# Kernel optimization log

Hardware: AMD Instinct MI355X
Metric: run time of the kernel (lower is better)

## Reference

```python
import jax, jax.numpy as jnp
import numpy as np

B, L, D, Y = 8, 2500, 512, 8921


def setup_inputs() -> dict:
    key = jax.random.key(0)
    k1, k2, k3, k4, k5, k6 = jax.random.split(key, 6)
    x = jax.random.normal(k1, (B, L, D), dtype=jnp.float32)
    target = jax.random.uniform(k2, (B, Y), dtype=jnp.float32)
    text_inputs = jax.random.randint(k3, (B, L), 0, 50000, dtype=jnp.int32)
    # Xavier-uniform-like init for the two [Y, D] weights
    lim = float(np.sqrt(6.0 / (Y + D)))
    U_weight = jax.random.uniform(k4, (Y, D), dtype=jnp.float32, minval=-lim, maxval=lim)
    final_weight = jax.random.uniform(k5, (Y, D), dtype=jnp.float32, minval=-lim, maxval=lim)
    final_bias = jax.random.uniform(k6, (Y,), dtype=jnp.float32, minval=-0.05, maxval=0.05)
    return {"x": x, "target": target, "text_inputs": text_inputs,
            "U_weight": U_weight, "final_weight": final_weight, "final_bias": final_bias}


def reference(x, target, text_inputs, U_weight, final_weight, final_bias):
    # att: [B, Y, L] = U.weight @ x^T
    att = jnp.einsum('yd,bld->byl', U_weight, x)
    # softmax over sequence dim
    alpha = jax.nn.softmax(att, axis=2)
    # per-label context: [B, Y, D]
    m = jnp.einsum('byl,bld->byd', alpha, x)
    # gated reduction instead of a linear layer: [B, Y]
    y = jnp.einsum('byd,yd->by', m, final_weight) + final_bias
    # BCEWithLogitsLoss (mean over all elements), numerically stable
    loss = jnp.mean(jnp.maximum(y, 0.0) - y * target + jnp.log1p(jnp.exp(-jnp.abs(y))))
    return (y, loss)
```

## Files before the change

kernel.cpp:

```cpp
#include <hip/hip_runtime.h>
#include <stdint.h>

#define B_ 8
#define L_ 2500
#define D_ 512
#define Y_ 8921
#define LP 2560
#define YP 8960
#define BLK 128
#define BK 32
#define NKT 16
#define NS 4
#define LTS 5

typedef float f32x4 __attribute__((ext_vector_type(4)));
typedef __bf16 bf16x8 __attribute__((ext_vector_type(8)));
typedef unsigned short u16;
typedef unsigned int u32;

__device__ __forceinline__ u32 pack2(float a, float b) {
  u32 ua = __float_as_uint(a); ua = (ua + 0x7FFFu + ((ua >> 16) & 1u)) >> 16;
  u32 ub = __float_as_uint(b); ub = (ub + 0x7FFFu + ((ub >> 16) & 1u)) >> 16;
  return ua | (ub << 16);
}

__global__ void cvt_x_kernel(const float* __restrict__ x, u16* __restrict__ xb) {
  int idx = blockIdx.x * 256 + threadIdx.x;
  int row = idx >> 6;
  int c8  = (idx & 63) << 3;
  int b = row / LP;
  int l = row - b * LP;
  uint4 o;
  if (l < L_) {
    const float* s = x + (size_t)(b * L_ + l) * D_ + c8;
    float4 f0 = *(const float4*)s;
    float4 f1 = *(const float4*)(s + 4);
    o.x = pack2(f0.x, f0.y); o.y = pack2(f0.z, f0.w);
    o.z = pack2(f1.x, f1.y); o.w = pack2(f1.z, f1.w);
  } else {
    o = make_uint4(0u, 0u, 0u, 0u);
  }
  *(uint4*)(xb + (size_t)row * D_ + c8) = o;
}

__global__ void cvt_w_kernel(const float* __restrict__ U, const float* __restrict__ Wf,
                             u16* __restrict__ Ub, u16* __restrict__ Wb) {
  int idx = blockIdx.x * 256 + threadIdx.x;
  const int half = YP * 64;
  const float* src = U; u16* dst = Ub;
  int i = idx;
  if (idx >= half) { i -= half; src = Wf; dst = Wb; }
  int row = i >> 6;
  int c8  = (i & 63) << 3;
  uint4 o;
  if (row < Y_) {
    const float* s = src + (size_t)row * D_ + c8;
    float4 f0 = *(const float4*)s;
    float4 f1 = *(const float4*)(s + 4);
    o.x = pack2(f0.x, f0.y); o.y = pack2(f0.z, f0.w);
    o.z = pack2(f1.x, f1.y); o.w = pack2(f1.z, f1.w);
  } else {
    o = make_uint4(0u, 0u, 0u, 0u);
  }
  *(uint4*)(dst + (size_t)row * D_ + c8) = o;
}

__device__ __forceinline__ void async16(const u16* g, u16* l) {
  __builtin_amdgcn_global_load_lds(
      (const __attribute__((address_space(1))) u32*)g,
      (__attribute__((address_space(3))) u32*)l, 16, 0, 0);
}

__global__ __launch_bounds__(256, 2) void fused_kernel(
    const u16* __restrict__ xb,
    const u16* __restrict__ Ub,
    const u16* __restrict__ Wb,
    float* __restrict__ part)
{
  __shared__ __align__(16) u16 sU[BLK * BK];
  __shared__ __align__(16) u16 sW[BLK * BK];
  __shared__ __align__(16) u16 sX[BLK * BK];

  const int t    = threadIdx.x;
  const int lane = t & 63;
  const int wv   = t >> 6;
  const int l16  = lane & 15;
  const int q    = lane >> 4;
  const int b    = blockIdx.y;
  const int y0   = blockIdx.x * BLK;
  const int s    = blockIdx.z;

  const int srow = t >> 2;
  const int scol = (t & 3) << 3;
  const u16* gU0 = Ub + (size_t)(y0 + srow) * D_ + scol;
  const u16* gU1 = gU0 + (size_t)64 * D_;
  const u16* gW0 = Wb + (size_t)(y0 + srow) * D_ + scol;
  const u16* gW1 = gW0 + (size_t)64 * D_;
  const u16* gXb = xb + (size_t)b * LP * D_ + (size_t)srow * D_ + scol;
  u16* lU0 = sU + t * 8;  u16* lU1 = sU + 2048 + t * 8;
  u16* lW0 = sW + t * 8;  u16* lW1 = sW + 2048 + t * 8;
  u16* lX0 = sX + t * 8;  u16* lX1 = sX + 2048 + t * 8;

  float M[8], Z[8], W[8];
#pragma unroll
  for (int i = 0; i < 8; ++i) { M[i] = -1e30f; Z[i] = 0.f; W[i] = 0.f; }

  const f32x4 z4 = {0.f, 0.f, 0.f, 0.f};

  for (int ltl = 0; ltl < LTS; ++ltl) {
    const int l0 = (s * LTS + ltl) * BLK;
    const u16* gX0 = gXb + (size_t)l0 * D_;
    const u16* gX1 = gX0 + (size_t)64 * D_;

    f32x4 accA[2][8], accS[2][8];
#pragma unroll
    for (int ry = 0; ry < 2; ++ry)
#pragma unroll
      for (int cl = 0; cl < 8; ++cl) { accA[ry][cl] = z4; accS[ry][cl] = z4; }

    for (int kt = 0; kt < NKT; ++kt) {
      const int ko = kt * BK;
      __syncthreads();
      async16(gU0 + ko, lU0);
      async16(gU1 + ko, lU1);
      async16(gW0 + ko, lW0);
      async16(gW1 + ko, lW1);
      async16(gX0 + ko, lX0);
      async16(gX1 + ko, lX1);
      __syncthreads();

      bf16x8 aU0 = *(const bf16x8*)(const void*)(sU + (wv * 32 + l16) * BK + q * 8);
      bf16x8 aU1 = *(const bf16x8*)(const void*)(sU + (wv * 32 + 16 + l16) * BK + q * 8);
      bf16x8 aW0 = *(const bf16x8*)(const void*)(sW + (wv * 32 + l16) * BK + q * 8);
      bf16x8 aW1 = *(const bf16x8*)(const void*)(sW + (wv * 32 + 16 + l16) * BK + q * 8);
#pragma unroll
      for (int cl = 0; cl < 8; ++cl) {
        bf16x8 bX = *(const bf16x8*)(const void*)(sX + (cl * 16 + l16) * BK + q * 8);
        accA[0][cl] = __builtin_amdgcn_mfma_f32_16x16x32_bf16(aU0, bX, accA[0][cl], 0, 0, 0);
        accA[1][cl] = __builtin_amdgcn_mfma_f32_16x16x32_bf16(aU1, bX, accA[1][cl], 0, 0, 0);
        accS[0][cl] = __builtin_amdgcn_mfma_f32_16x16x32_bf16(aW0, bX, accS[0][cl], 0, 0, 0);
        accS[1][cl] = __builtin_amdgcn_mfma_f32_16x16x32_bf16(aW1, bX, accS[1][cl], 0, 0, 0);
      }
    }

    const bool boundary = (l0 + BLK > L_);
#pragma unroll
    for (int ry = 0; ry < 2; ++ry) {
#pragma unroll
      for (int r = 0; r < 4; ++r) {
        const int si = ry * 4 + r;
        float a[8];
        if (boundary) {
#pragma unroll
          for (int cl = 0; cl < 8; ++cl) {
            float v = accA[ry][cl][r];
            a[cl] = (l0 + cl * 16 + l16 >= L_) ? -1e30f : v;
          }
        } else {
#pragma unroll
          for (int cl = 0; cl < 8; ++cl) a[cl] = accA[ry][cl][r];
        }
        float tmax = a[0];
#pragma unroll
        for (int cl = 1; cl < 8; ++cl) tmax = fmaxf(tmax, a[cl]);
        const float mnew  = fmaxf(M[si], tmax);
        const float scale = __expf(M[si] - mnew);
        float zl = 0.f, wl = 0.f;
#pragma unroll
        for (int cl = 0; cl < 8; ++cl) {
          float p = __expf(a[cl] - mnew);
          zl += p;
          wl = fmaf(p, accS[ry][cl][r], wl);
        }
        Z[si] = fmaf(Z[si], scale, zl);
        W[si] = fmaf(W[si], scale, wl);
        M[si] = mnew;
      }
    }
  }

#pragma unroll
  for (int si = 0; si < 8; ++si) {
    float M0 = M[si], Z0 = Z[si], W0 = W[si];
#pragma unroll
    for (int st = 1; st <= 8; st <<= 1) {
      const float Mo = __shfl_xor(M0, st);
      const float Zo = __shfl_xor(Z0, st);
      const float Wo = __shfl_xor(W0, st);
      const float mn = fmaxf(M0, Mo);
      const float sa = __expf(M0 - mn);
      const float sb = __expf(Mo - mn);
      Z0 = Z0 * sa + Zo * sb;
      W0 = W0 * sa + Wo * sb;
      M0 = mn;
    }
    M[si] = M0; Z[si] = Z0; W[si] = W0;
  }

  if (l16 == 0) {
    float* p = part + ((size_t)(b * 70 + blockIdx.x) * NS + s) * 384;
#pragma unroll
    for (int ry = 0; ry < 2; ++ry) {
#pragma unroll
      for (int r = 0; r < 4; ++r) {
        const int si = ry * 4 + r;
        const int yl = wv * 32 + ry * 16 + q * 4 + r;
        p[yl]       = M[si];
        p[128 + yl] = Z[si];
        p[256 + yl] = W[si];
      }
    }
  }
}

__global__ void combine_kernel(const float* __restrict__ part,
                               const float* __restrict__ bias,
                               const float* __restrict__ target,
                               float* __restrict__ out) {
  const int idx = blockIdx.x * 256 + threadIdx.x;
  float lpart = 0.f;
  if (idx < B_ * Y_) {
    const int b = idx / Y_;
    const int y = idx - b * Y_;
    const int yt = y >> 7, yl = y & 127;
    const float* p = part + ((size_t)(b * 70 + yt) * NS) * 384 + yl;
    float M = -1e30f;
#pragma unroll
    for (int s2 = 0; s2 < NS; ++s2) M = fmaxf(M, p[s2 * 384]);
    float Z = 0.f, W = 0.f;
#pragma unroll
    for (int s2 = 0; s2 < NS; ++s2) {
      const float e = __expf(p[s2 * 384] - M);
      Z = fmaf(p[s2 * 384 + 128], e, Z);
      W = fmaf(p[s2 * 384 + 256], e, W);
    }
    const float yv = W / Z + bias[y];
    out[idx] = yv;
    const float tg = target[idx];
    lpart = fmaxf(yv, 0.f) - yv * tg + log1pf(__expf(-fabsf(yv)));
  }
  lpart += __shfl_xor(lpart, 1);  lpart += __shfl_xor(lpart, 2);
  lpart += __shfl_xor(lpart, 4);  lpart += __shfl_xor(lpart, 8);
  lpart += __shfl_xor(lpart, 16); lpart += __shfl_xor(lpart, 32);
  if ((threadIdx.x & 63) == 0)
    atomicAdd(out + (size_t)B_ * Y_, lpart * (1.0f / (B_ * Y_)));
}

extern "C" void kernel_launch(void* const* d_in, const int* in_sizes, int n_in,
                              void* d_out, int out_size, void* d_ws, size_t ws_size,
                              hipStream_t stream) {
  const float* x      = (const float*)d_in[0];
  const float* target = (const float*)d_in[1];
  const float* U      = (const float*)d_in[3];
  const float* Wf     = (const float*)d_in[4];
  const float* bias   = (const float*)d_in[5];
  float* out = (float*)d_out;

  u16* xb = (u16*)d_ws;
  u16* Ub = xb + (size_t)B_ * LP * D_;
  u16* Wb = Ub + (size_t)YP * D_;
  float* part = (float*)(Wb + (size_t)YP * D_);

  hipMemsetAsync(out + (size_t)B_ * Y_, 0, sizeof(float), stream);
  cvt_x_kernel<<<dim3((B_ * LP * 64) / 256), 256, 0, stream>>>(x, xb);
  cvt_w_kernel<<<dim3((2 * YP * 64) / 256), 256, 0, stream>>>(U, Wf, Ub, Wb);
  fused_kernel<<<dim3(YP / BLK, B_, NS), 256, 0, stream>>>(xb, Ub, Wb, part);
  combine_kernel<<<dim3((B_ * Y_ + 255) / 256), 256, 0, stream>>>(part, bias, target, out);
}
```

Before: 575.7 us.

## Double-buffer LDS tiles and prefetch next k-step across sequence tiles

Shared-memory tiles for U, W and x are doubled. Each iteration issues the async global-to-LDS loads for the next k-step, which can cross into the next sequence tile, before computing on the current buffer. A manual vmcnt wait and barriers replace the two syncthreads per step, and MFMA sections run at raised wave priority. The aim is to hide global load latency behind the matrix math, at the cost of twice the LDS footprint, which may reduce occupancy.

```diff
diff --git a/kernel.cpp b/kernel.cpp
--- a/kernel.cpp
+++ b/kernel.cpp
@@ -12,6 +12,7 @@
 #define NKT 16
 #define NS 4
 #define LTS 5
+#define TOT (LTS * NKT)
 
 typedef float f32x4 __attribute__((ext_vector_type(4)));
 typedef __bf16 bf16x8 __attribute__((ext_vector_type(8)));
@@ -77,9 +78,9 @@
     const u16* __restrict__ Wb,
     float* __restrict__ part)
 {
-  __shared__ __align__(16) u16 sU[BLK * BK];
-  __shared__ __align__(16) u16 sW[BLK * BK];
-  __shared__ __align__(16) u16 sX[BLK * BK];
+  __shared__ __align__(16) u16 sU[2][BLK * BK];
+  __shared__ __align__(16) u16 sW[2][BLK * BK];
+  __shared__ __align__(16) u16 sX[2][BLK * BK];
 
   const int t    = threadIdx.x;
   const int lane = t & 63;
@@ -97,9 +98,6 @@
   const u16* gW0 = Wb + (size_t)(y0 + srow) * D_ + scol;
   const u16* gW1 = gW0 + (size_t)64 * D_;
   const u16* gXb = xb + (size_t)b * LP * D_ + (size_t)srow * D_ + scol;
-  u16* lU0 = sU + t * 8;  u16* lU1 = sU + 2048 + t * 8;
-  u16* lW0 = sW + t * 8;  u16* lW1 = sW + 2048 + t * 8;
-  u16* lX0 = sX + t * 8;  u16* lX1 = sX + 2048 + t * 8;
 
   float M[8], Z[8], W[8];
 #pragma unroll
@@ -107,42 +105,62 @@
 
   const f32x4 z4 = {0.f, 0.f, 0.f, 0.f};
 
+  auto stage = [&](int stp, int bf) {
+    const int kt = stp & (NKT - 1);
+    const int lt = stp >> 4;
+    const int ko = kt * BK;
+    const u16* gX = gXb + (size_t)((s * LTS + lt) * BLK) * D_ + ko;
+    async16(gU0 + ko, &sU[bf][t * 8]);
+    async16(gU1 + ko, &sU[bf][2048 + t * 8]);
+    async16(gW0 + ko, &sW[bf][t * 8]);
+    async16(gW1 + ko, &sW[bf][2048 + t * 8]);
+    async16(gX,                  &sX[bf][t * 8]);
+    async16(gX + (size_t)64 * D_, &sX[bf][2048 + t * 8]);
+  };
+
+  stage(0, 0);
+
+  int step = 0;
   for (int ltl = 0; ltl < LTS; ++ltl) {
+    f32x4 accA[2][8], accS[2][8];
+#pragma unroll
+    for (int ry = 0; ry < 2; ++ry)
+#pragma unroll
+      for (int cl = 0; cl < 8; ++cl) { accA[ry][cl] = z4; accS[ry][cl] = z4; }
+
+    for (int kt = 0; kt < NKT; ++kt, ++step) {
+      const int nstep = step + 1;
+      if (nstep < TOT) stage(nstep, nstep & 1);
+
+      if (nstep < TOT) asm volatile("s_waitcnt vmcnt(6)" ::: "memory");
+      else             asm volatile("s_waitcnt vmcnt(0)" ::: "memory");
+      __builtin_amdgcn_s_barrier();
+      asm volatile("" ::: "memory");
+
+      const int cb = step & 1;
+      const u16* bU = sU[cb];
+      const u16* bW = sW[cb];
+      const u16* bX = sX[cb];
+
+      bf16x8 aU0 = *(const bf16x8*)(const void*)(bU + (wv * 32 + l16) * BK + q * 8);
+      bf16x8 aU1 = *(const bf16x8*)(const void*)(bU + (wv * 32 + 16 + l16) * BK + q * 8);
+      bf16x8 aW0 = *(const bf16x8*)(const void*)(bW + (wv * 32 + l16) * BK + q * 8);
+      bf16x8 aW1 = *(const bf16x8*)(const void*)(bW + (wv * 32 + 16 + l16) * BK + q * 8);
+      __builtin_amdgcn_s_setprio(1);
+#pragma unroll
+      for (int cl = 0; cl < 8; ++cl) {
+        bf16x8 bXf = *(const bf16x8*)(const void*)(bX + (cl * 16 + l16) * BK + q * 8);
+        accA[0][cl] = __builtin_amdgcn_mfma_f32_16x16x32_bf16(aU0, bXf, accA[0][cl], 0, 0, 0);
+        accA[1][cl] = __builtin_amdgcn_mfma_f32_16x16x32_bf16(aU1, bXf, accA[1][cl], 0, 0, 0);
+        accS[0][cl] = __builtin_amdgcn_mfma_f32_16x16x32_bf16(aW0, bXf, accS[0][cl], 0, 0, 0);
+        accS[1][cl] = __builtin_amdgcn_mfma_f32_16x16x32_bf16(aW1, bXf, accS[1][cl], 0, 0, 0);
+      }
+      __builtin_amdgcn_s_setprio(0);
+      asm volatile("" ::: "memory");
+      __builtin_amdgcn_s_barrier();
+    }
+
     const int l0 = (s * LTS + ltl) * BLK;
-    const u16* gX0 = gXb + (size_t)l0 * D_;
-    const u16* gX1 = gX0 + (size_t)64 * D_;
-
-    f32x4 accA[2][8], accS[2][8];
-#pragma unroll
-    for (int ry = 0; ry < 2; ++ry)
-#pragma unroll
-      for (int cl = 0; cl < 8; ++cl) { accA[ry][cl] = z4; accS[ry][cl] = z4; }
-
-    for (int kt = 0; kt < NKT; ++kt) {
-      const int ko = kt * BK;
-      __syncthreads();
-      async16(gU0 + ko, lU0);
-      async16(gU1 + ko, lU1);
-      async16(gW0 + ko, lW0);
-      async16(gW1 + ko, lW1);
-      async16(gX0 + ko, lX0);
-      async16(gX1 + ko, lX1);
-      __syncthreads();
-
-      bf16x8 aU0 = *(const bf16x8*)(const void*)(sU + (wv * 32 + l16) * BK + q * 8);
-      bf16x8 aU1 = *(const bf16x8*)(const void*)(sU + (wv * 32 + 16 + l16) * BK + q * 8);
-      bf16x8 aW0 = *(const bf16x8*)(const void*)(sW + (wv * 32 + l16) * BK + q * 8);
-      bf16x8 aW1 = *(const bf16x8*)(const void*)(sW + (wv * 32 + 16 + l16) * BK + q * 8);
-#pragma unroll
-      for (int cl = 0; cl < 8; ++cl) {
-        bf16x8 bX = *(const bf16x8*)(const void*)(sX + (cl * 16 + l16) * BK + q * 8);
-        accA[0][cl] = __builtin_amdgcn_mfma_f32_16x16x32_bf16(aU0, bX, accA[0][cl], 0, 0, 0);
-        accA[1][cl] = __builtin_amdgcn_mfma_f32_16x16x32_bf16(aU1, bX, accA[1][cl], 0, 0, 0);
-        accS[0][cl] = __builtin_amdgcn_mfma_f32_16x16x32_bf16(aW0, bX, accS[0][cl], 0, 0, 0);
-        accS[1][cl] = __builtin_amdgcn_mfma_f32_16x16x32_bf16(aW1, bX, accS[1][cl], 0, 0, 0);
-      }
-    }
-
     const bool boundary = (l0 + BLK > L_);
 #pragma unroll
     for (int ry = 0; ry < 2; ++ry) {
```

Result: no change. 585.8 us (+1.7%).

## Load U/W fragments directly from global and double K-step per barrier

Applied to the files above, without the earlier changes.

U and W weight fragments are now read straight from global memory into registers instead of being staged through shared memory. Only x is staged, with two 32-wide K slices per barrier pair, which halves the synchronizations and cuts LDS footprint. The trade-off is repeated global/L2 reads of U/W per L tile (five per block) with no LDS reuse, and more exposed global-load latency before the MFMAs.

```diff
diff --git a/kernel.cpp b/kernel.cpp
--- a/kernel.cpp
+++ b/kernel.cpp
@@ -9,7 +9,7 @@
 #define YP 8960
 #define BLK 128
 #define BK 32
-#define NKT 16
+#define NST 8
 #define NS 4
 #define LTS 5
 
@@ -77,9 +77,7 @@
     const u16* __restrict__ Wb,
     float* __restrict__ part)
 {
-  __shared__ __align__(16) u16 sU[BLK * BK];
-  __shared__ __align__(16) u16 sW[BLK * BK];
-  __shared__ __align__(16) u16 sX[BLK * BK];
+  __shared__ __align__(16) u16 sX[2 * BLK * BK];
 
   const int t    = threadIdx.x;
   const int lane = t & 63;
@@ -92,14 +90,10 @@
 
   const int srow = t >> 2;
   const int scol = (t & 3) << 3;
-  const u16* gU0 = Ub + (size_t)(y0 + srow) * D_ + scol;
-  const u16* gU1 = gU0 + (size_t)64 * D_;
-  const u16* gW0 = Wb + (size_t)(y0 + srow) * D_ + scol;
-  const u16* gW1 = gW0 + (size_t)64 * D_;
   const u16* gXb = xb + (size_t)b * LP * D_ + (size_t)srow * D_ + scol;
-  u16* lU0 = sU + t * 8;  u16* lU1 = sU + 2048 + t * 8;
-  u16* lW0 = sW + t * 8;  u16* lW1 = sW + 2048 + t * 8;
-  u16* lX0 = sX + t * 8;  u16* lX1 = sX + 2048 + t * 8;
+
+  const u16* fU = Ub + (size_t)(y0 + wv * 32 + l16) * D_ + q * 8;
+  const u16* fW = Wb + (size_t)(y0 + wv * 32 + l16) * D_ + q * 8;
 
   float M[8], Z[8], W[8];
 #pragma unroll
@@ -118,28 +112,32 @@
 #pragma unroll
       for (int cl = 0; cl < 8; ++cl) { accA[ry][cl] = z4; accS[ry][cl] = z4; }
 
-    for (int kt = 0; kt < NKT; ++kt) {
-      const int ko = kt * BK;
+#pragma unroll
+    for (int st = 0; st < NST; ++st) {
+      const int kb = st * 64;
       __syncthreads();
-      async16(gU0 + ko, lU0);
-      async16(gU1 + ko, lU1);
-      async16(gW0 + ko, lW0);
-      async16(gW1 + ko, lW1);
-      async16(gX0 + ko, lX0);
-      async16(gX1 + ko, lX1);
+      async16(gX0 + kb,      sX + t * 8);
+      async16(gX1 + kb,      sX + 2048 + t * 8);
+      async16(gX0 + kb + 32, sX + 4096 + t * 8);
+      async16(gX1 + kb + 32, sX + 4096 + 2048 + t * 8);
       __syncthreads();
 
-      bf16x8 aU0 = *(const bf16x8*)(const void*)(sU + (wv * 32 + l16) * BK + q * 8);
-      bf16x8 aU1 = *(const bf16x8*)(const void*)(sU + (wv * 32 + 16 + l16) * BK + q * 8);
-      bf16x8 aW0 = *(const bf16x8*)(const void*)(sW + (wv * 32 + l16) * BK + q * 8);
-      bf16x8 aW1 = *(const bf16x8*)(const void*)(sW + (wv * 32 + 16 + l16) * BK + q * 8);
-#pragma unroll
-      for (int cl = 0; cl < 8; ++cl) {
-        bf16x8 bX = *(const bf16x8*)(const void*)(sX + (cl * 16 + l16) * BK + q * 8);
-        accA[0][cl] = __builtin_amdgcn_mfma_f32_16x16x32_bf16(aU0, bX, accA[0][cl], 0, 0, 0);
-        accA[1][cl] = __builtin_amdgcn_mfma_f32_16x16x32_bf16(aU1, bX, accA[1][cl], 0, 0, 0);
-        accS[0][cl] = __builtin_amdgcn_mfma_f32_16x16x32_bf16(aW0, bX, accS[0][cl], 0, 0, 0);
-        accS[1][cl] = __builtin_amdgcn_mfma_f32_16x16x32_bf16(aW1, bX, accS[1][cl], 0, 0, 0);
+#pragma unroll
+      for (int kk = 0; kk < 2; ++kk) {
+        const int kt = st * 2 + kk;
+        bf16x8 aU0 = *(const bf16x8*)(const void*)(fU + kt * 32);
+        bf16x8 aU1 = *(const bf16x8*)(const void*)(fU + 16 * D_ + kt * 32);
+        bf16x8 aW0 = *(const bf16x8*)(const void*)(fW + kt * 32);
+        bf16x8 aW1 = *(const bf16x8*)(const void*)(fW + 16 * D_ + kt * 32);
+        const u16* bXb = sX + kk * 4096;
+#pragma unroll
+        for (int cl = 0; cl < 8; ++cl) {
+          bf16x8 bX = *(const bf16x8*)(const void*)(bXb + (cl * 16 + l16) * BK + q * 8);
+          accA[0][cl] = __builtin_amdgcn_mfma_f32_16x16x32_bf16(aU0, bX, accA[0][cl], 0, 0, 0);
+          accA[1][cl] = __builtin_amdgcn_mfma_f32_16x16x32_bf16(aU1, bX, accA[1][cl], 0, 0, 0);
+          accS[0][cl] = __builtin_amdgcn_mfma_f32_16x16x32_bf16(aW0, bX, accS[0][cl], 0, 0, 0);
+          accS[1][cl] = __builtin_amdgcn_mfma_f32_16x16x32_bf16(aW1, bX, accS[1][cl], 0, 0, 0);
+        }
       }
     }
 
```

Measured after the change: 880.7 us. 53.0% more time.

## Load U/W fragments directly from global and remap blocks for XCD locality

Applied to the files above, without the earlier changes.

The U and W operand fragments are now read straight from global memory into registers rather than staged through shared memory, which drops two LDS buffers and four async copies per k-step. The grid is flattened to 1D and remapped so that consecutive work items (same y-tile, all batches and splits) land on the same XCD, improving L2 reuse of the U/W tiles. The cost is uncoalesced-ish direct global loads that are reloaded for each L tile, with latency now sitting in front of the barrier.

```diff
diff --git a/kernel.cpp b/kernel.cpp
--- a/kernel.cpp
+++ b/kernel.cpp
@@ -12,6 +12,8 @@
 #define NKT 16
 #define NS 4
 #define LTS 5
+#define NBLK (70 * B_ * NS)
+#define PERX (NBLK / 8)
 
 typedef float f32x4 __attribute__((ext_vector_type(4)));
 typedef __bf16 bf16x8 __attribute__((ext_vector_type(8)));
@@ -77,8 +79,6 @@
     const u16* __restrict__ Wb,
     float* __restrict__ part)
 {
-  __shared__ __align__(16) u16 sU[BLK * BK];
-  __shared__ __align__(16) u16 sW[BLK * BK];
   __shared__ __align__(16) u16 sX[BLK * BK];
 
   const int t    = threadIdx.x;
@@ -86,20 +86,25 @@
   const int wv   = t >> 6;
   const int l16  = lane & 15;
   const int q    = lane >> 4;
-  const int b    = blockIdx.y;
-  const int y0   = blockIdx.x * BLK;
-  const int s    = blockIdx.z;
+
+  const int bid = blockIdx.x;
+  const int w   = (bid & 7) * PERX + (bid >> 3);
+  const int yt  = w >> 5;
+  const int rem = w & 31;
+  const int b   = rem >> 2;
+  const int s   = rem & 3;
+  const int y0  = yt * BLK;
 
   const int srow = t >> 2;
   const int scol = (t & 3) << 3;
-  const u16* gU0 = Ub + (size_t)(y0 + srow) * D_ + scol;
-  const u16* gU1 = gU0 + (size_t)64 * D_;
-  const u16* gW0 = Wb + (size_t)(y0 + srow) * D_ + scol;
-  const u16* gW1 = gW0 + (size_t)64 * D_;
   const u16* gXb = xb + (size_t)b * LP * D_ + (size_t)srow * D_ + scol;
-  u16* lU0 = sU + t * 8;  u16* lU1 = sU + 2048 + t * 8;
-  u16* lW0 = sW + t * 8;  u16* lW1 = sW + 2048 + t * 8;
-  u16* lX0 = sX + t * 8;  u16* lX1 = sX + 2048 + t * 8;
+  u16* lX0 = sX + t * 8;
+  u16* lX1 = sX + 2048 + t * 8;
+
+  const u16* fU0 = Ub + (size_t)(y0 + wv * 32 + l16) * D_ + q * 8;
+  const u16* fU1 = fU0 + (size_t)16 * D_;
+  const u16* fW0 = Wb + (size_t)(y0 + wv * 32 + l16) * D_ + q * 8;
+  const u16* fW1 = fW0 + (size_t)16 * D_;
 
   float M[8], Z[8], W[8];
 #pragma unroll
@@ -118,21 +123,18 @@
 #pragma unroll
       for (int cl = 0; cl < 8; ++cl) { accA[ry][cl] = z4; accS[ry][cl] = z4; }
 
+#pragma unroll 1
     for (int kt = 0; kt < NKT; ++kt) {
       const int ko = kt * BK;
+      bf16x8 aU0 = *(const bf16x8*)(const void*)(fU0 + ko);
+      bf16x8 aU1 = *(const bf16x8*)(const void*)(fU1 + ko);
+      bf16x8 aW0 = *(const bf16x8*)(const void*)(fW0 + ko);
+      bf16x8 aW1 = *(const bf16x8*)(const void*)(fW1 + ko);
       __syncthreads();
-      async16(gU0 + ko, lU0);
-      async16(gU1 + ko, lU1);
-      async16(gW0 + ko, lW0);
-      async16(gW1 + ko, lW1);
       async16(gX0 + ko, lX0);
       async16(gX1 + ko, lX1);
       __syncthreads();
 
-      bf16x8 aU0 = *(const bf16x8*)(const void*)(sU + (wv * 32 + l16) * BK + q * 8);
-      bf16x8 aU1 = *(const bf16x8*)(const void*)(sU + (wv * 32 + 16 + l16) * BK + q * 8);
-      bf16x8 aW0 = *(const bf16x8*)(const void*)(sW + (wv * 32 + l16) * BK + q * 8);
-      bf16x8 aW1 = *(const bf16x8*)(const void*)(sW + (wv * 32 + 16 + l16) * BK + q * 8);
 #pragma unroll
       for (int cl = 0; cl < 8; ++cl) {
         bf16x8 bX = *(const bf16x8*)(const void*)(sX + (cl * 16 + l16) * BK + q * 8);
@@ -198,7 +200,7 @@
   }
 
   if (l16 == 0) {
-    float* p = part + ((size_t)(b * 70 + blockIdx.x) * NS + s) * 384;
+    float* p = part + ((size_t)(b * 70 + yt) * NS + s) * 384;
 #pragma unroll
     for (int ry = 0; ry < 2; ++ry) {
 #pragma unroll
@@ -264,6 +266,6 @@
   hipMemsetAsync(out + (size_t)B_ * Y_, 0, sizeof(float), stream);
   cvt_x_kernel<<<dim3((B_ * LP * 64) / 256), 256, 0, stream>>>(x, xb);
   cvt_w_kernel<<<dim3((2 * YP * 64) / 256), 256, 0, stream>>>(U, Wf, Ub, Wb);
-  fused_kernel<<<dim3(YP / BLK, B_, NS), 256, 0, stream>>>(xb, Ub, Wb, part);
+  fused_kernel<<<dim3(NBLK), 256, 0, stream>>>(xb, Ub, Wb, part);
   combine_kernel<<<dim3((B_ * Y_ + 255) / 256), 256, 0, stream>>>(part, bias, target, out);
 }
```

Result: slower. 604.0 us (+4.9%).
